# Kernel optimization log

Measured on AMD Instinct MI355X. Metric: run time of the kernel, lower is better.

## Reference

```python
import jax, jax.numpy as jnp
import numpy as np

ALPHA = 0.2          # LeakyReLU negative slope
NEG_CAP = -9e15      # clamp used by the original torch.where on log(adj)


def setup_inputs() -> dict:
    key = jax.random.key(0)
    B, C, V, L, H, E = 4, 32, 1000, 12, 4, 20000
    k1, k2, k3, k4 = jax.random.split(key, 4)
    x = jax.random.normal(k1, (B, C, V, L), dtype=jnp.float32)
    # xavier_uniform-like scale with gain 1.414 (use normal for simplicity of stats)
    W = jax.random.normal(k2, (H, C, C), dtype=jnp.float32) * np.float32(1.414 * np.sqrt(2.0 / (C + C)))
    a = jax.random.normal(k3, (H, 2 * C, 1), dtype=jnp.float32) * np.float32(1.414 * np.sqrt(2.0 / (2 * C + 1)))
    # edge list: V self-loops (every row nonempty -> rowsum > 0) + random edges
    rng = np.random.default_rng(0)
    src = np.concatenate([np.arange(V), rng.integers(0, V, E - V)]).astype(np.int64)
    dst = np.concatenate([np.arange(V), rng.integers(0, V, E - V)]).astype(np.int64)
    edge_index = jnp.asarray(np.stack([src, dst]))           # [2, E]
    # edge_val = adj[edge0, edge1]; positive so log() is finite
    edge_val = jax.random.uniform(k4, (E,), dtype=jnp.float32, minval=0.05, maxval=1.0)
    return {"x": x, "W": W, "a": a, "edge_index": edge_index, "edge_val": edge_val}


def reference(x, W, a, edge_index, edge_val):
    # x: [B,C,V,L], W: [H,C,C], a: [H,2C,1], edge_index: [2,E], edge_val: [E]
    H, C = W.shape[0], W.shape[2]
    V = x.shape[2]
    e0, e1 = edge_index[0], edge_index[1]

    # h = einsum('ncvl,hcd->hndvl'): [H,B,C,V,L]
    h = jnp.einsum('bcvl,hcd->hbdvl', x, W)

    # attention score: a applied to cat(h[src], h[dst]) == a_src.h[src] + a_dst.h[dst]
    a_src, a_dst = a[:, :C, 0], a[:, C:, 0]                   # [H,C]
    s_src = jnp.einsum('hbcvl,hc->hbvl', h, a_src)            # [H,B,V,L]
    s_dst = jnp.einsum('hbcvl,hc->hbvl', h, a_dst)
    score = s_src[:, :, e0, :] + s_dst[:, :, e1, :]           # [H,B,E,L]

    edge_e = jnp.exp(-jax.nn.leaky_relu(score, ALPHA))        # [H,B,E,L]
    lv = jnp.maximum(jnp.log(edge_val), NEG_CAP)              # [E]
    edge_e = edge_e * lv[None, None, :, None]
    # (dropout is identity in eval mode)

    # e_rowsum: sparse [V,V] @ ones -> per-row sum, scatter by e0: [V,H,B,L]
    rowsum = jax.ops.segment_sum(jnp.moveaxis(edge_e, 2, 0), e0, num_segments=V)

    # h_prime numerator: scatter (edge_e * h[dst]) by e0
    hg = h[:, :, :, e1, :]                                    # [H,B,C,E,L]
    msg = edge_e[:, :, None, :, :] * hg                       # [H,B,C,E,L]
    num = jax.ops.segment_sum(jnp.moveaxis(msg, 3, 0), e0, num_segments=V)  # [V,H,B,C,L]

    h_prime = num / rowsum[:, :, :, None, :]                  # [V,H,B,C,L]
    h_avg = jnp.mean(h_prime, axis=1)                         # [V,B,C,L]
    out = jnp.transpose(h_avg, (1, 2, 0, 3))                  # [B,C,V,L]
    return jax.nn.elu(out)
```

## Files before the change

kernel.cpp:

```cpp
#include <hip/hip_runtime.h>
#include <hip/hip_bf16.h>
#include <hip/hip_fp16.h>
#include <math.h>

#define HH 4
#define BB 4
#define CC 32
#define VV 1000
#define LL 12
#define EE 20000
#define NBL (BB * LL)
#define SS (HH * NBL)
#define RCAP 128
#define LALPHA 0.2f
#define NEG_CAP_F -9000000000000000.0f

typedef unsigned int uint;
typedef unsigned short ushort;

__global__ __launch_bounds__(256) void k_h(const float* __restrict__ x,
                                           const float* __restrict__ W,
                                           const float* __restrict__ a,
                                           ushort* __restrict__ h_g,
                                           float* __restrict__ s_src,
                                           float* __restrict__ s_dst,
                                           int* __restrict__ cnt,
                                           const int* __restrict__ ei,
                                           const float* __restrict__ ev,
                                           uint2* __restrict__ csr) {
  if (blockIdx.x >= 500) {
    int e = ((blockIdx.x - 500) * 4 + blockIdx.y) * 256 + threadIdx.x;
    if (e < EE) {
      int r = ei[e];
      int d = ei[EE + e];
      int pos = atomicAdd(&cnt[r], 1);
      if (pos < RCAP) {
        float lv = fmaxf(__logf(ev[e]), NEG_CAP_F);
        csr[r * RCAP + pos] = make_uint2((uint)d, __float_as_uint(lv));
      }
    }
    return;
  }

  __shared__ float W_lds[HH * CC * CC];
  __shared__ float a_lds[HH * 2 * CC];
  __shared__ float x_s[CC * 2 * LL];
  __shared__ float wa[HH][2][CC];
  const int tid = threadIdx.x;
  const int b = blockIdx.y;
  const int v0 = blockIdx.x * 2;

  {
    const float4* Wf = (const float4*)W;
    float4* Wl = (float4*)W_lds;
    for (int i = tid; i < HH * CC * CC / 4; i += 256) Wl[i] = Wf[i];
  }
  a_lds[tid] = a[tid];
#pragma unroll
  for (int k = 0; k < 3; ++k) {
    int i = k * 256 + tid;
    int ci = i / 24, r = i - ci * 24;
    x_s[i] = x[(b * CC + ci) * (VV * LL) + v0 * LL + r];
  }
  __syncthreads();

  {
    int h = tid >> 6, which = (tid >> 5) & 1, ci = tid & 31;
    float acc = 0.f;
#pragma unroll
    for (int k = 0; k < CC; ++k) {
      int c = (k + ci) & 31;
      acc = fmaf(W_lds[h * CC * CC + ci * CC + c],
                 a_lds[h * 2 * CC + which * CC + c], acc);
    }
    wa[h][which][ci] = acc;
  }
  __syncthreads();

  const int vp = tid >> 7;
  const int h = (tid >> 5) & 3;
  const int c = tid & 31;
  const int v = v0 + vp;

  int xoff = (b * CC) * (VV * LL) + v * LL;
  xoff = __builtin_amdgcn_readfirstlane(xoff);
  const float* xr = x + xoff;

  float acc[LL];
#pragma unroll
  for (int l = 0; l < LL; ++l) acc[l] = 0.f;

#pragma unroll 4
  for (int ci = 0; ci < CC; ++ci) {
    float w = W_lds[h * CC * CC + ci * CC + c];
#pragma unroll
    for (int l = 0; l < LL; ++l)
      acc[l] = fmaf(xr[ci * (VV * LL) + l], w, acc[l]);
  }

  const int slab0 = h * NBL + b * LL;
#pragma unroll
  for (int l = 0; l < LL; ++l) {
    __half hv = __float2half(acc[l]);
    h_g[((size_t)(slab0 + l) * VV + v) * CC + c] = *(ushort*)&hv;
  }

  if (tid < 192) {
    int which = tid & 1;
    int t2 = tid >> 1;
    int l = t2 % 12;
    int h2 = (t2 / 12) & 3;
    int vp2 = t2 / 48;
    float s = 0.f;
#pragma unroll
    for (int ci = 0; ci < CC; ++ci)
      s = fmaf(x_s[ci * 24 + vp2 * 12 + l], wa[h2][which][ci], s);
    int slab = h2 * NBL + b * LL + l;
    float* dp = which ? s_dst : s_src;
    dp[slab * VV + v0 + vp2] = s;
  }
}

__global__ __launch_bounds__(256) void k_agg(const ushort* __restrict__ hg,
                                             const float* __restrict__ s_src,
                                             const float* __restrict__ s_dst,
                                             const int* __restrict__ cnt,
                                             const uint2* __restrict__ csr,
                                             float* __restrict__ outp) {
  const int i = blockIdx.x;
  const int xcd = i & 7;
  const int q = i >> 3;
  const int bl = xcd * 6 + q / 250;
  const int vb = q % 250;
  const int warp = threadIdx.x >> 6;
  const int v = vb * 4 + warp;
  const int lane = threadIdx.x & 63;
  const int b = bl / LL, l = bl - b * LL;

  int deg = cnt[v];
  if (deg > RCAP) deg = RCAP;
  const int rbase = v * RCAP;

  const int ii = lane >> 4;
  const int h = (lane >> 2) & 3;
  const int cg = lane & 3;

  const int slabB = h * NBL + bl;
  const float ssv = s_src[slabB * VV + v];
  const float* sdb = s_dst + slabB * VV;
  const uint hoff = (uint)(slabB * (VV * CC * 2)) + (uint)(cg * 16);
  const char* hgbytes = (const char*)hg;

  float num[8];
#pragma unroll
  for (int j = 0; j < 8; ++j) num[j] = 0.f;
  float rs = 0.f;

  for (int e = ii; e < deg; e += 4) {
    uint2 ent = csr[rbase + e];
    uint d = ent.x;
    float lv = __uint_as_float(ent.y);
    float s = ssv + sdb[d];
    float lr = fmaxf(s, LALPHA * s);
    float ee = __expf(-lr) * lv;
    uint voff = (d << 6) + hoff;
    uint4 g = *(const uint4*)(hgbytes + voff);
    __half2 p0 = __builtin_bit_cast(__half2, g.x);
    __half2 p1 = __builtin_bit_cast(__half2, g.y);
    __half2 p2 = __builtin_bit_cast(__half2, g.z);
    __half2 p3 = __builtin_bit_cast(__half2, g.w);
    num[0] = fmaf(ee, __low2float(p0), num[0]);
    num[1] = fmaf(ee, __high2float(p0), num[1]);
    num[2] = fmaf(ee, __low2float(p1), num[2]);
    num[3] = fmaf(ee, __high2float(p1), num[3]);
    num[4] = fmaf(ee, __low2float(p2), num[4]);
    num[5] = fmaf(ee, __high2float(p2), num[5]);
    num[6] = fmaf(ee, __low2float(p3), num[6]);
    num[7] = fmaf(ee, __high2float(p3), num[7]);
    rs += ee;
  }

#pragma unroll
  for (int mm = 16; mm <= 32; mm <<= 1) {
#pragma unroll
    for (int j = 0; j < 8; ++j) num[j] += __shfl_xor(num[j], mm);
    rs += __shfl_xor(rs, mm);
  }
  float inv = __frcp_rn(rs);
  float val[8];
#pragma unroll
  for (int j = 0; j < 8; ++j) val[j] = num[j] * inv;
#pragma unroll
  for (int mm = 4; mm <= 8; mm <<= 1) {
#pragma unroll
    for (int j = 0; j < 8; ++j) val[j] += __shfl_xor(val[j], mm);
  }

  if (ii == 0) {
    int j0 = 2 * h;
    float a0 = val[j0] * 0.25f;
    float a1 = val[j0 + 1] * 0.25f;
    a0 = a0 > 0.f ? a0 : expm1f(a0);
    a1 = a1 > 0.f ? a1 : expm1f(a1);
    size_t o0 = ((size_t)(b * CC + cg * 8 + j0) * VV + v) * LL + l;
    outp[o0] = a0;
    outp[o0 + (size_t)VV * LL] = a1;
  }
}

extern "C" void kernel_launch(void* const* d_in, const int* in_sizes, int n_in,
                              void* d_out, int out_size, void* d_ws, size_t ws_size,
                              hipStream_t stream) {
  const float* x = (const float*)d_in[0];
  const float* W = (const float*)d_in[1];
  const float* a = (const float*)d_in[2];
  const int* ei = (const int*)d_in[3];
  const float* ev = (const float*)d_in[4];
  float* out = (float*)d_out;
  float* ws = (float*)d_ws;

  size_t o = 0;
  ushort* h_g = (ushort*)(ws + o);  o += (size_t)SS * VV * CC / 2;
  float* s_src = ws + o;            o += SS * VV;
  float* s_dst = ws + o;            o += SS * VV;
  int* cnt = (int*)(ws + o);        o += 1024;
  uint2* csr = (uint2*)(ws + o);    o += (size_t)VV * RCAP * 2;

  hipMemsetAsync(cnt, 0, 1024 * sizeof(int), stream);

  dim3 gA(520, BB);
  k_h<<<gA, 256, 0, stream>>>(x, W, a, h_g, s_src, s_dst, cnt, ei, ev, csr);

  k_agg<<<12000, 256, 0, stream>>>(h_g, s_src, s_dst, cnt, csr, out);
}
```

Measured before the change: 65.18 us.

## Interleave heads in h and score layouts, process two nodes and two edges per warp

Stores h as [B*L, V, H*C] and the scores as [B*L, V, H], so all four heads of a gathered destination node sit in one contiguous 256-byte row. A warp's gather for one edge then touches a single cache region instead of four separate slabs. The aggregation kernel now handles two nodes per warp at half the block count, and each lane unrolls two edges per iteration so more loads are in flight. The costs are a strided store pattern in the producer kernel and extra predication for odd edge counts.

Measured after the change: 59.17 us. -9.2%, faster.

```diff
diff --git a/kernel.cpp b/kernel.cpp
--- a/kernel.cpp
+++ b/kernel.cpp
@@ -21,9 +21,9 @@
 __global__ __launch_bounds__(256) void k_h(const float* __restrict__ x,
                                            const float* __restrict__ W,
                                            const float* __restrict__ a,
-                                           ushort* __restrict__ h_g,
-                                           float* __restrict__ s_src,
-                                           float* __restrict__ s_dst,
+                                           ushort* __restrict__ hg2,
+                                           float* __restrict__ s_src2,
+                                           float* __restrict__ s_dst2,
                                            int* __restrict__ cnt,
                                            const int* __restrict__ ei,
                                            const float* __restrict__ ev,
@@ -98,11 +98,11 @@
       acc[l] = fmaf(xr[ci * (VV * LL) + l], w, acc[l]);
   }
 
-  const int slab0 = h * NBL + b * LL;
 #pragma unroll
   for (int l = 0; l < LL; ++l) {
     __half hv = __float2half(acc[l]);
-    h_g[((size_t)(slab0 + l) * VV + v) * CC + c] = *(ushort*)&hv;
+    hg2[((size_t)((b * LL + l) * VV) + v) * (HH * CC) + h * CC + c] =
+        *(ushort*)&hv;
   }
 
   if (tid < 192) {
@@ -115,96 +115,120 @@
 #pragma unroll
     for (int ci = 0; ci < CC; ++ci)
       s = fmaf(x_s[ci * 24 + vp2 * 12 + l], wa[h2][which][ci], s);
-    int slab = h2 * NBL + b * LL + l;
-    float* dp = which ? s_dst : s_src;
-    dp[slab * VV + v0 + vp2] = s;
+    float* dp = which ? s_dst2 : s_src2;
+    dp[((size_t)((b * LL + l) * VV) + v0 + vp2) * HH + h2] = s;
   }
 }
 
-__global__ __launch_bounds__(256) void k_agg(const ushort* __restrict__ hg,
-                                             const float* __restrict__ s_src,
-                                             const float* __restrict__ s_dst,
+__global__ __launch_bounds__(256) void k_agg(const ushort* __restrict__ hg2,
+                                             const float* __restrict__ s_src2,
+                                             const float* __restrict__ s_dst2,
                                              const int* __restrict__ cnt,
                                              const uint2* __restrict__ csr,
                                              float* __restrict__ outp) {
   const int i = blockIdx.x;
   const int xcd = i & 7;
-  const int q = i >> 3;
-  const int bl = xcd * 6 + q / 250;
-  const int vb = q % 250;
+  const int j = i >> 3;
+  const int bl = xcd * 6 + j / 125;
+  const int vb = j % 125;
   const int warp = threadIdx.x >> 6;
-  const int v = vb * 4 + warp;
   const int lane = threadIdx.x & 63;
   const int b = bl / LL, l = bl - b * LL;
-
-  int deg = cnt[v];
-  if (deg > RCAP) deg = RCAP;
-  const int rbase = v * RCAP;
 
   const int ii = lane >> 4;
   const int h = (lane >> 2) & 3;
   const int cg = lane & 3;
 
-  const int slabB = h * NBL + bl;
-  const float ssv = s_src[slabB * VV + v];
-  const float* sdb = s_dst + slabB * VV;
-  const uint hoff = (uint)(slabB * (VV * CC * 2)) + (uint)(cg * 16);
-  const char* hgbytes = (const char*)hg;
-
-  float num[8];
-#pragma unroll
-  for (int j = 0; j < 8; ++j) num[j] = 0.f;
-  float rs = 0.f;
-
-  for (int e = ii; e < deg; e += 4) {
-    uint2 ent = csr[rbase + e];
-    uint d = ent.x;
-    float lv = __uint_as_float(ent.y);
-    float s = ssv + sdb[d];
-    float lr = fmaxf(s, LALPHA * s);
-    float ee = __expf(-lr) * lv;
-    uint voff = (d << 6) + hoff;
-    uint4 g = *(const uint4*)(hgbytes + voff);
-    __half2 p0 = __builtin_bit_cast(__half2, g.x);
-    __half2 p1 = __builtin_bit_cast(__half2, g.y);
-    __half2 p2 = __builtin_bit_cast(__half2, g.z);
-    __half2 p3 = __builtin_bit_cast(__half2, g.w);
-    num[0] = fmaf(ee, __low2float(p0), num[0]);
-    num[1] = fmaf(ee, __high2float(p0), num[1]);
-    num[2] = fmaf(ee, __low2float(p1), num[2]);
-    num[3] = fmaf(ee, __high2float(p1), num[3]);
-    num[4] = fmaf(ee, __low2float(p2), num[4]);
-    num[5] = fmaf(ee, __high2float(p2), num[5]);
-    num[6] = fmaf(ee, __low2float(p3), num[6]);
-    num[7] = fmaf(ee, __high2float(p3), num[7]);
-    rs += ee;
-  }
-
-#pragma unroll
-  for (int mm = 16; mm <= 32; mm <<= 1) {
-#pragma unroll
-    for (int j = 0; j < 8; ++j) num[j] += __shfl_xor(num[j], mm);
-    rs += __shfl_xor(rs, mm);
-  }
-  float inv = __frcp_rn(rs);
-  float val[8];
-#pragma unroll
-  for (int j = 0; j < 8; ++j) val[j] = num[j] * inv;
-#pragma unroll
-  for (int mm = 4; mm <= 8; mm <<= 1) {
-#pragma unroll
-    for (int j = 0; j < 8; ++j) val[j] += __shfl_xor(val[j], mm);
-  }
-
-  if (ii == 0) {
-    int j0 = 2 * h;
-    float a0 = val[j0] * 0.25f;
-    float a1 = val[j0 + 1] * 0.25f;
-    a0 = a0 > 0.f ? a0 : expm1f(a0);
-    a1 = a1 > 0.f ? a1 : expm1f(a1);
-    size_t o0 = ((size_t)(b * CC + cg * 8 + j0) * VV + v) * LL + l;
-    outp[o0] = a0;
-    outp[o0 + (size_t)VV * LL] = a1;
+  const float* ssb = s_src2 + (size_t)bl * VV * HH;
+  const float* sdb = s_dst2 + (size_t)bl * VV * HH;
+  const char* hgbytes = (const char*)hg2 + (size_t)bl * VV * (HH * CC * 2);
+  const uint hoff = (uint)(h * (CC * 2)) + (uint)(cg * 16);
+
+#pragma unroll
+  for (int k = 0; k < 2; ++k) {
+    const int v = vb * 8 + warp * 2 + k;
+    int deg = cnt[v];
+    if (deg > RCAP) deg = RCAP;
+    const int rbase = v * RCAP;
+    const float ssv = ssb[v * HH + h];
+
+    float num[8];
+#pragma unroll
+    for (int q = 0; q < 8; ++q) num[q] = 0.f;
+    float rs = 0.f;
+
+    for (int e = 2 * ii; e < deg; e += 8) {
+      int e1 = e + 1;
+      int e1c = e1 < deg ? e1 : e;
+      uint2 entA = csr[rbase + e];
+      uint2 entB = csr[rbase + e1c];
+      uint dA = entA.x, dB = entB.x;
+      float sdA = sdb[dA * HH + h];
+      float sdB = sdb[dB * HH + h];
+      uint4 gA = *(const uint4*)(hgbytes + ((dA << 8) + hoff));
+      uint4 gB = *(const uint4*)(hgbytes + ((dB << 8) + hoff));
+
+      float sA = ssv + sdA;
+      float lrA = fmaxf(sA, LALPHA * sA);
+      float eeA = __expf(-lrA) * __uint_as_float(entA.y);
+      float sB = ssv + sdB;
+      float lrB = fmaxf(sB, LALPHA * sB);
+      float eeB = __expf(-lrB) * __uint_as_float(entB.y);
+      eeB = (e1 < deg) ? eeB : 0.f;
+
+      __half2 a0 = __builtin_bit_cast(__half2, gA.x);
+      __half2 a1 = __builtin_bit_cast(__half2, gA.y);
+      __half2 a2 = __builtin_bit_cast(__half2, gA.z);
+      __half2 a3 = __builtin_bit_cast(__half2, gA.w);
+      num[0] = fmaf(eeA, __low2float(a0), num[0]);
+      num[1] = fmaf(eeA, __high2float(a0), num[1]);
+      num[2] = fmaf(eeA, __low2float(a1), num[2]);
+      num[3] = fmaf(eeA, __high2float(a1), num[3]);
+      num[4] = fmaf(eeA, __low2float(a2), num[4]);
+      num[5] = fmaf(eeA, __high2float(a2), num[5]);
+      num[6] = fmaf(eeA, __low2float(a3), num[6]);
+      num[7] = fmaf(eeA, __high2float(a3), num[7]);
+      __half2 b0 = __builtin_bit_cast(__half2, gB.x);
+      __half2 b1 = __builtin_bit_cast(__half2, gB.y);
+      __half2 b2 = __builtin_bit_cast(__half2, gB.z);
+      __half2 b3 = __builtin_bit_cast(__half2, gB.w);
+      num[0] = fmaf(eeB, __low2float(b0), num[0]);
+      num[1] = fmaf(eeB, __high2float(b0), num[1]);
+      num[2] = fmaf(eeB, __low2float(b1), num[2]);
+      num[3] = fmaf(eeB, __high2float(b1), num[3]);
+      num[4] = fmaf(eeB, __low2float(b2), num[4]);
+      num[5] = fmaf(eeB, __high2float(b2), num[5]);
+      num[6] = fmaf(eeB, __low2float(b3), num[6]);
+      num[7] = fmaf(eeB, __high2float(b3), num[7]);
+      rs += eeA + eeB;
+    }
+
+#pragma unroll
+    for (int mm = 16; mm <= 32; mm <<= 1) {
+#pragma unroll
+      for (int q = 0; q < 8; ++q) num[q] += __shfl_xor(num[q], mm);
+      rs += __shfl_xor(rs, mm);
+    }
+    float inv = __frcp_rn(rs);
+    float val[8];
+#pragma unroll
+    for (int q = 0; q < 8; ++q) val[q] = num[q] * inv;
+#pragma unroll
+    for (int mm = 4; mm <= 8; mm <<= 1) {
+#pragma unroll
+      for (int q = 0; q < 8; ++q) val[q] += __shfl_xor(val[q], mm);
+    }
+
+    if (ii == 0) {
+      int j0 = 2 * h;
+      float a0 = val[j0] * 0.25f;
+      float a1 = val[j0 + 1] * 0.25f;
+      a0 = a0 > 0.f ? a0 : expm1f(a0);
+      a1 = a1 > 0.f ? a1 : expm1f(a1);
+      size_t o0 = ((size_t)(b * CC + cg * 8 + j0) * VV + v) * LL + l;
+      outp[o0] = a0;
+      outp[o0 + (size_t)VV * LL] = a1;
+    }
   }
 }
 
@@ -220,16 +244,16 @@
   float* ws = (float*)d_ws;
 
   size_t o = 0;
-  ushort* h_g = (ushort*)(ws + o);  o += (size_t)SS * VV * CC / 2;
-  float* s_src = ws + o;            o += SS * VV;
-  float* s_dst = ws + o;            o += SS * VV;
+  ushort* hg2 = (ushort*)(ws + o);  o += (size_t)NBL * VV * (HH * CC) / 2;
+  float* s_src2 = ws + o;           o += (size_t)NBL * VV * HH;
+  float* s_dst2 = ws + o;           o += (size_t)NBL * VV * HH;
   int* cnt = (int*)(ws + o);        o += 1024;
   uint2* csr = (uint2*)(ws + o);    o += (size_t)VV * RCAP * 2;
 
   hipMemsetAsync(cnt, 0, 1024 * sizeof(int), stream);
 
   dim3 gA(520, BB);
-  k_h<<<gA, 256, 0, stream>>>(x, W, a, h_g, s_src, s_dst, cnt, ei, ev, csr);
-
-  k_agg<<<12000, 256, 0, stream>>>(h_g, s_src, s_dst, cnt, csr, out);
+  k_h<<<gA, 256, 0, stream>>>(x, W, a, hg2, s_src2, s_dst2, cnt, ei, ev, csr);
+
+  k_agg<<<6000, 256, 0, stream>>>(hg2, s_src2, s_dst2, cnt, csr, out);
 }
```
